# Kernel tuning notes

Measured on AMD Instinct MI355X. Metric: run time of the kernel, lower is better.

## Reference

```python
import jax, jax.numpy as jnp
import numpy as np

B, T, D, H, HD, E, F, K = 512, 32, 512, 16, 32, 4, 2048, 2
EPS = 1e-5

def gelu_gpt2(x):
    c = np.sqrt(2.0 / np.pi).astype(np.float32)
    return 0.5 * x * (1.0 + jnp.tanh(c * (x + 0.044715 * x ** 3)))

def layernorm(x, g, b):
    m = jnp.mean(x, axis=-1, keepdims=True)
    v = jnp.mean((x - m) ** 2, axis=-1, keepdims=True)
    return (x - m) * jax.lax.rsqrt(v + EPS) * g + b

def setup_inputs() -> dict:
    key = jax.random.key(0)
    ks = jax.random.split(key, 12)
    s = 0.02
    return {
        "x": jax.random.normal(ks[0], (B, T, D), jnp.float32),
        "ln1_g": jnp.ones((D,), jnp.float32), "ln1_b": jnp.zeros((D,), jnp.float32),
        "wq": jax.random.normal(ks[1], (H, D, HD), jnp.float32) * s,
        "wk": jax.random.normal(ks[2], (H, D, HD), jnp.float32) * s,
        "wv": jax.random.normal(ks[3], (H, D, HD), jnp.float32) * s,
        "w_proj": jax.random.normal(ks[4], (D, D), jnp.float32) * s,
        "b_proj": jnp.zeros((D,), jnp.float32),
        "ln2_g": jnp.ones((D,), jnp.float32), "ln2_b": jnp.zeros((D,), jnp.float32),
        "w_gate": jax.random.normal(ks[5], (D, E), jnp.float32) * s,
        "w1": jax.random.normal(ks[6], (E, D, F), jnp.float32) * s,
        "b1": jnp.zeros((E, F), jnp.float32),
        "w2": jax.random.normal(ks[7], (E, F, D), jnp.float32) * s,
        "b2": jnp.zeros((E, D), jnp.float32),
    }

def reference(x, ln1_g, ln1_b, wq, wk, wv, w_proj, b_proj, ln2_g, ln2_b, w_gate, w1, b1, w2, b2):
    # --- multi-head causal attention (dropout = eval-mode identity) ---
    h = layernorm(x, ln1_g, ln1_b)                       # [B,T,D]
    q = jnp.einsum('btd,hde->bhte', h, wq)
    k = jnp.einsum('btd,hde->bhte', h, wk)
    v = jnp.einsum('btd,hde->bhte', h, wv)
    # NOTE: original scales by 1/sqrt(n_embd), not head_size
    wei = jnp.einsum('bhte,bhse->bhts', q, k) / jnp.sqrt(jnp.float32(D))
    mask = jnp.tril(jnp.ones((T, T), bool))
    wei = jnp.where(mask, wei, -jnp.inf)
    wei = jax.nn.softmax(wei, axis=-1)
    att = jnp.einsum('bhts,bhse->bhte', wei, v)          # [B,H,T,HD]
    att = att.transpose(0, 2, 1, 3).reshape(B, T, D)     # concat heads
    x = x + att @ w_proj + b_proj
    # --- mixture of experts FFN ---
    h2 = layernorm(x, ln2_g, ln2_b).reshape(-1, D)       # [N,D]
    logits = h2 @ w_gate                                  # [N,E] raw gate output
    # faithful to original: scalar mean over all logits
    ep = jnp.mean(logits)
    bal_loss = ep * jnp.log(ep + 0.1)
    w_top, sel = jax.lax.top_k(logits, K)                # [N,K]
    w_top = jax.nn.softmax(w_top, axis=-1)
    combine = jnp.sum(w_top[:, :, None] * jax.nn.one_hot(sel, E, dtype=x.dtype), axis=1)  # [N,E]
    mid = gelu_gpt2(jnp.einsum('nd,edf->nef', h2, w1) + b1)   # [N,E,F]
    eout = jnp.einsum('nef,efd->ned', mid, w2) + b2           # [N,E,D]
    moe = jnp.einsum('ne,ned->nd', combine, eout).reshape(B, T, D)
    return (x + moe, bal_loss)
```

## Files before the change

### kernel.cpp

```cpp
#include <hip/hip_runtime.h>

typedef unsigned short ushort;
typedef unsigned int   uint;
typedef short bf16x8 __attribute__((ext_vector_type(8)));
typedef float f32x4  __attribute__((ext_vector_type(4)));

__device__ __forceinline__ float bf2f(ushort u){
  union { uint u; float f; } c; c.u = ((uint)u) << 16; return c.f;
}
__device__ __forceinline__ ushort f2bf(float f){
  union { float f; uint u; } c; c.f = f;
  return (ushort)((c.u + 0x7fffu + ((c.u >> 16) & 1u)) >> 16);
}
__device__ __forceinline__ float wredsum(float v){
  #pragma unroll
  for (int off = 32; off > 0; off >>= 1) v += __shfl_xor(v, off);
  return v;
}
__device__ __forceinline__ void gload16(const void* g, void* l){
  __builtin_amdgcn_global_load_lds((__attribute__((address_space(1))) void*)(void*)g,
                                   (__attribute__((address_space(3))) void*)l, 16, 0, 0);
}

template<bool SPLIT>
__global__ __launch_bounds__(256) void transpose_to_bf16(
    const float* __restrict__ src, ushort* __restrict__ dhi, ushort* __restrict__ dlo,
    int R, int C)
{
  __shared__ float tile[32][33];
  size_t zoff = (size_t)blockIdx.z * R * C;
  src += zoff; dhi += zoff; if (SPLIT) dlo += zoff;
  int c0 = blockIdx.x * 32, r0 = blockIdx.y * 32;
  int tx = threadIdx.x & 31, ty = threadIdx.x >> 5;
  #pragma unroll
  for (int i = 0; i < 32; i += 8)
    tile[ty + i][tx] = src[(size_t)(r0 + ty + i) * C + (c0 + tx)];
  __syncthreads();
  #pragma unroll
  for (int i = 0; i < 32; i += 8){
    float v = tile[tx][ty + i];
    ushort hi = f2bf(v);
    dhi[(size_t)(c0 + ty + i) * R + (r0 + tx)] = hi;
    if constexpr (SPLIT)
      dlo[(size_t)(c0 + ty + i) * R + (r0 + tx)] = f2bf(v - bf2f(hi));
  }
}

__global__ __launch_bounds__(256) void ln_split(
    const float* __restrict__ x, const float* __restrict__ g, const float* __restrict__ b,
    ushort* __restrict__ hhi, ushort* __restrict__ hlo)
{
  int w = threadIdx.x >> 6, lane = threadIdx.x & 63;
  int row = blockIdx.x * 4 + w;
  const float* xr = x + (size_t)row * 512;
  int d = lane * 8;
  float4 a0 = *(const float4*)(xr + d);
  float4 a1 = *(const float4*)(xr + d + 4);
  float v[8] = {a0.x,a0.y,a0.z,a0.w,a1.x,a1.y,a1.z,a1.w};
  float s = 0.f;
  #pragma unroll
  for (int j = 0; j < 8; j++) s += v[j];
  s = wredsum(s);
  float mean = s * (1.f/512.f);
  float q = 0.f;
  #pragma unroll
  for (int j = 0; j < 8; j++){ float t = v[j] - mean; q += t*t; }
  q = wredsum(q);
  float rstd = rsqrtf(q * (1.f/512.f) + 1e-5f);
  ushort hu[8], lu[8];
  #pragma unroll
  for (int j = 0; j < 8; j++){
    float h = (v[j] - mean) * rstd * g[d+j] + b[d+j];
    ushort hi = f2bf(h);
    hu[j] = hi;
    lu[j] = f2bf(h - bf2f(hi));
  }
  uint4 oh, ol;
  oh.x = (uint)hu[0] | ((uint)hu[1]<<16); oh.y = (uint)hu[2] | ((uint)hu[3]<<16);
  oh.z = (uint)hu[4] | ((uint)hu[5]<<16); oh.w = (uint)hu[6] | ((uint)hu[7]<<16);
  ol.x = (uint)lu[0] | ((uint)lu[1]<<16); ol.y = (uint)lu[2] | ((uint)lu[3]<<16);
  ol.z = (uint)lu[4] | ((uint)lu[5]<<16); ol.w = (uint)lu[6] | ((uint)lu[7]<<16);
  *(uint4*)(hhi + (size_t)row*512 + d) = oh;
  *(uint4*)(hlo + (size_t)row*512 + d) = ol;
}

template<int EP>
__global__ __launch_bounds__(256) void gemm_bt(
    const ushort* __restrict__ A, const ushort* __restrict__ Alo,
    const ushort* __restrict__ B, const ushort* __restrict__ Blo,
    int M, int N, int K,
    float* __restrict__ outF,
    const float* __restrict__ bias, const float* __restrict__ resid)
{
  __shared__ __align__(16) ushort As[2][128*32];
  __shared__ __align__(16) ushort Bs[2][128*32];
  const int tid  = threadIdx.x;
  const int lane = tid & 63;
  const int w    = tid >> 6;
  const int wm   = w >> 1, wn = w & 1;
  const int bm   = blockIdx.x, bn = blockIdx.y;

  const int    srow = w*16 + (lane >> 2);
  const int    scol = (lane & 3) * 8;
  const size_t aoff = (size_t)(bm*128 + srow) * K + scol;
  const size_t boff = (size_t)(bn*128 + srow) * K + scol;
  const int lbase0 = (w*16) * 32;
  const int lbase1 = (64 + w*16) * 32;

  f32x4 acc[4][4];
  #pragma unroll
  for (int i = 0; i < 4; i++)
    #pragma unroll
    for (int j = 0; j < 4; j++) acc[i][j] = f32x4{0.f,0.f,0.f,0.f};

  const int nk = K >> 5;
  for (int kt = 0; kt < nk; ++kt) {
    const size_t ko = (size_t)kt * 32;
    gload16(A + aoff + ko,               &As[0][lbase0]);
    gload16(A + aoff + (size_t)64*K + ko,&As[0][lbase1]);
    gload16(B + boff + ko,               &Bs[0][lbase0]);
    gload16(B + boff + (size_t)64*K + ko,&Bs[0][lbase1]);
    gload16(Alo + aoff + ko,               &As[1][lbase0]);
    gload16(Alo + aoff + (size_t)64*K + ko,&As[1][lbase1]);
    gload16(Blo + boff + ko,               &Bs[1][lbase0]);
    gload16(Blo + boff + (size_t)64*K + ko,&Bs[1][lbase1]);
    __syncthreads();

    bf16x8 ah[4], bh[4], al[4], bl[4];
    const int kk = (lane >> 4) * 8;
    const int ar = wm*64 + (lane & 15);
    const int br = wn*64 + (lane & 15);
    #pragma unroll
    for (int i = 0; i < 4; i++){
      ah[i] = *(const bf16x8*)&As[0][(ar + i*16)*32 + kk];
      bh[i] = *(const bf16x8*)&Bs[0][(br + i*16)*32 + kk];
      al[i] = *(const bf16x8*)&As[1][(ar + i*16)*32 + kk];
      bl[i] = *(const bf16x8*)&Bs[1][(br + i*16)*32 + kk];
    }
    #pragma unroll
    for (int i = 0; i < 4; i++)
      #pragma unroll
      for (int j = 0; j < 4; j++){
        acc[i][j] = __builtin_amdgcn_mfma_f32_16x16x32_bf16(ah[i], bh[j], acc[i][j], 0,0,0);
        acc[i][j] = __builtin_amdgcn_mfma_f32_16x16x32_bf16(ah[i], bl[j], acc[i][j], 0,0,0);
        acc[i][j] = __builtin_amdgcn_mfma_f32_16x16x32_bf16(al[i], bh[j], acc[i][j], 0,0,0);
      }
    __syncthreads();
  }

  const int r0 = bm*128 + wm*64;
  const int c0 = bn*128 + wn*64;
  const int cl = lane & 15;
  const int rl = (lane >> 4) * 4;
  #pragma unroll
  for (int i = 0; i < 4; i++){
    #pragma unroll
    for (int r = 0; r < 4; r++){
      const int row = r0 + i*16 + rl + r;
      #pragma unroll
      for (int j = 0; j < 4; j++){
        const int col = c0 + j*16 + cl;
        float v = acc[i][j][r];
        size_t idx = (size_t)row * N + col;
        if constexpr (EP == 0) outF[idx] = v;
        else                   outF[idx] = v + bias[col] + resid[idx];
      }
    }
  }
}

__global__ __launch_bounds__(256) void gemm_w1(
    const ushort* __restrict__ A, const ushort* __restrict__ Ball,
    const float* __restrict__ biasAll, ushort* __restrict__ midOut,
    const int* __restrict__ list, const int* __restrict__ seg)
{
  constexpr int K = 512, N = 2048, NBN = 16;
  __shared__ __align__(16) ushort LB[128*132];
  const int tid = threadIdx.x, lane = tid & 63, w = tid >> 6;
  const int wm = w >> 1, wn = w & 1;

  const int nloc = gridDim.x >> 3;
  const int lid  = (blockIdx.x & 7) * nloc + (blockIdx.x >> 3);
  const int bm   = lid / NBN, bn = lid % NBN;
  if (bm >= seg[4]) return;
  int e = 0;
  while (bm >= seg[e+1]) e++;
  const int ltile = bm - seg[e];
  const int* listE = list + e*16384;

  const int jrows = w * 32;
  const int lrow  = lane >> 3;
  const int lgcol = (((lane & 7) ^ lrow)) * 8;

  size_t asrc[4], bsrc[4];
  const ushort* Bm = Ball + (size_t)e * N * K;
  #pragma unroll
  for (int j = 0; j < 4; j++){
    int ar8 = jrows + j*8 + lrow;
    int tok = listE[ltile*128 + ar8];
    asrc[j] = (size_t)tok * K + lgcol;
    bsrc[j] = (size_t)(bn*128 + ar8) * K + lgcol;
  }

  f32x4 acc[4][4];
  #pragma unroll
  for (int i = 0; i < 4; i++)
    #pragma unroll
    for (int j = 0; j < 4; j++) acc[i][j] = f32x4{0.f,0.f,0.f,0.f};

  const int ar = wm*64 + (lane & 15);
  const int br = wn*64 + (lane & 15);
  const int rsw = lane & 7;

  #pragma unroll
  for (int kt = 0; kt < (K >> 6); ++kt){
    const size_t k0 = (size_t)kt * 64;
    #pragma unroll
    for (int j = 0; j < 4; j++){
      gload16(A  + asrc[j] + k0, &LB[(jrows + j*8)*64]);
      gload16(Bm + bsrc[j] + k0, &LB[8192 + (jrows + j*8)*64]);
    }
    __syncthreads();
    #pragma unroll
    for (int ks = 0; ks < 2; ++ks){
      const int g    = ks*4 + (lane >> 4);
      const int goff = (g ^ rsw) * 8;
      bf16x8 af[4], bfr[4];
      #pragma unroll
      for (int i = 0; i < 4; i++){
        af[i]  = *(const bf16x8*)&LB[(ar + i*16)*64 + goff];
        bfr[i] = *(const bf16x8*)&LB[8192 + (br + i*16)*64 + goff];
      }
      #pragma unroll
      for (int i = 0; i < 4; i++)
        #pragma unroll
        for (int j = 0; j < 4; j++)
          acc[i][j] = __builtin_amdgcn_mfma_f32_16x16x32_bf16(af[i], bfr[j], acc[i][j], 0,0,0);
    }
    __syncthreads();
  }

  const int cl = lane & 15;
  const int rl = (lane >> 4) * 4;
  float bj[4];
  #pragma unroll
  for (int j = 0; j < 4; j++)
    bj[j] = biasAll[e*N + bn*128 + wn*64 + j*16 + cl];
  #pragma unroll
  for (int i = 0; i < 4; i++){
    #pragma unroll
    for (int j = 0; j < 4; j++){
      const int cc = wn*64 + j*16 + cl;
      #pragma unroll
      for (int r = 0; r < 4; r++){
        const int rloc = wm*64 + i*16 + rl + r;
        float t = acc[i][j][r] + bj[j];
        float u2 = 1.5957691216057308f * (t + 0.044715f * t*t*t);
        float ex = __expf(u2);
        float gl = t - t * __builtin_amdgcn_rcpf(ex + 1.f);
        LB[rloc*132 + cc] = f2bf(gl);
      }
    }
  }
  __syncthreads();
  const int ch = tid & 15;
  #pragma unroll
  for (int it = 0; it < 8; ++it){
    const int rr = (tid >> 4) + it*16;
    bf16x8 v = *(const bf16x8*)&LB[rr*132 + ch*8];
    *(bf16x8*)&midOut[(size_t)(bm*128 + rr)*2048 + bn*128 + ch*8] = v;
  }
}

__global__ __launch_bounds__(256) void gemm_w2(
    const ushort* __restrict__ mid, const ushort* __restrict__ Ball,
    const float* __restrict__ biasAll, ushort* __restrict__ eout,
    const int* __restrict__ seg)
{
  constexpr int K = 2048, N = 512, NBN = 4;
  __shared__ __align__(16) ushort LB[4*128*64];
  const int tid = threadIdx.x, lane = tid & 63, w = tid >> 6;
  const int wm = w >> 1, wn = w & 1;

  const int nloc = gridDim.x >> 3;
  const int lid  = (blockIdx.x & 7) * nloc + (blockIdx.x >> 3);
  const int bm   = lid / NBN, bn = lid % NBN;
  if (bm >= seg[4]) return;
  int e = 0;
  while (bm >= seg[e+1]) e++;

  const int jrows = w * 32;
  const int lrow  = lane >> 3;
  const int lgcol = (((lane & 7) ^ lrow)) * 8;

  size_t asrc[4], bsrc[4];
  const ushort* Bm = Ball + (size_t)e * N * K;
  #pragma unroll
  for (int j = 0; j < 4; j++){
    int ar8 = jrows + j*8 + lrow;
    asrc[j] = (size_t)(bm*128 + ar8) * K + lgcol;
    bsrc[j] = (size_t)(bn*128 + ar8) * K + lgcol;
  }

  f32x4 acc[4][4];
  #pragma unroll
  for (int i = 0; i < 4; i++)
    #pragma unroll
    for (int j = 0; j < 4; j++) acc[i][j] = f32x4{0.f,0.f,0.f,0.f};

  constexpr int nk = K >> 6;

  #pragma unroll
  for (int j = 0; j < 4; j++){
    gload16(mid + asrc[j], &LB[(jrows + j*8)*64]);
    gload16(Bm  + bsrc[j], &LB[16384 + (jrows + j*8)*64]);
  }
  __syncthreads();

  const int ar = wm*64 + (lane & 15);
  const int br = wn*64 + (lane & 15);
  const int rsw = lane & 7;

  for (int kt = 0; kt < nk; ++kt){
    const int cur = kt & 1;
    const int curA = cur * 8192;
    const int nxtA = (cur ^ 1) * 8192;
    if (kt + 1 < nk){
      const size_t k0 = (size_t)(kt + 1) * 64;
      #pragma unroll
      for (int j = 0; j < 4; j++){
        gload16(mid + asrc[j] + k0, &LB[nxtA + (jrows + j*8)*64]);
        gload16(Bm  + bsrc[j] + k0, &LB[16384 + nxtA + (jrows + j*8)*64]);
      }
    }
    #pragma unroll
    for (int ks = 0; ks < 2; ++ks){
      const int g    = ks*4 + (lane >> 4);
      const int goff = (g ^ rsw) * 8;
      bf16x8 af[4], bfr[4];
      #pragma unroll
      for (int i = 0; i < 4; i++){
        af[i]  = *(const bf16x8*)&LB[curA + (ar + i*16)*64 + goff];
        bfr[i] = *(const bf16x8*)&LB[16384 + curA + (br + i*16)*64 + goff];
      }
      #pragma unroll
      for (int i = 0; i < 4; i++)
        #pragma unroll
        for (int j = 0; j < 4; j++)
          acc[i][j] = __builtin_amdgcn_mfma_f32_16x16x32_bf16(af[i], bfr[j], acc[i][j], 0,0,0);
    }
    __syncthreads();
  }

  const int cl = lane & 15;
  const int rl = (lane >> 4) * 4;
  float bj[4];
  #pragma unroll
  for (int j = 0; j < 4; j++)
    bj[j] = biasAll[e*N + bn*128 + wn*64 + j*16 + cl];
  #pragma unroll
  for (int i = 0; i < 4; i++){
    #pragma unroll
    for (int j = 0; j < 4; j++){
      const int cc = wn*64 + j*16 + cl;
      #pragma unroll
      for (int r = 0; r < 4; r++){
        const int rloc = wm*64 + i*16 + rl + r;
        LB[rloc*132 + cc] = f2bf(acc[i][j][r] + bj[j]);
      }
    }
  }
  __syncthreads();
  const int ch = tid & 15;
  #pragma unroll
  for (int it = 0; it < 8; ++it){
    const int rr = (tid >> 4) + it*16;
    bf16x8 v = *(const bf16x8*)&LB[rr*132 + ch*8];
    *(bf16x8*)&eout[(size_t)(bm*128 + rr)*512 + bn*128 + ch*8] = v;
  }
}

__global__ __launch_bounds__(256) void moe_combine(
    const ushort* __restrict__ eout, const int2* __restrict__ rowSlots,
    const float2* __restrict__ wts, float* __restrict__ out)
{
  int w = threadIdx.x >> 6, lane = threadIdx.x & 63;
  int row = blockIdx.x * 4 + w;
  int2 rs = rowSlots[row];
  float2 wv = wts[row];
  int d = lane * 8;
  uint4 u0 = *(const uint4*)(eout + (size_t)rs.x*512 + d);
  uint4 u1 = *(const uint4*)(eout + (size_t)rs.y*512 + d);
  float* op = out + (size_t)row*512 + d;
  float4 o0 = *(float4*)op;
  float4 o1 = *(float4*)(op + 4);
  o0.x += wv.x*bf2f((ushort)u0.x)        + wv.y*bf2f((ushort)u1.x);
  o0.y += wv.x*bf2f((ushort)(u0.x>>16))  + wv.y*bf2f((ushort)(u1.x>>16));
  o0.z += wv.x*bf2f((ushort)u0.y)        + wv.y*bf2f((ushort)u1.y);
  o0.w += wv.x*bf2f((ushort)(u0.y>>16))  + wv.y*bf2f((ushort)(u1.y>>16));
  o1.x += wv.x*bf2f((ushort)u0.z)        + wv.y*bf2f((ushort)u1.z);
  o1.y += wv.x*bf2f((ushort)(u0.z>>16))  + wv.y*bf2f((ushort)(u1.z>>16));
  o1.z += wv.x*bf2f((ushort)u0.w)        + wv.y*bf2f((ushort)u1.w);
  o1.w += wv.x*bf2f((ushort)(u0.w>>16))  + wv.y*bf2f((ushort)(u1.w>>16));
  *(float4*)op       = o0;
  *(float4*)(op + 4) = o1;
}

__global__ __launch_bounds__(64) void attn32(
    const float* __restrict__ qkv, ushort* __restrict__ atthi, ushort* __restrict__ attlo)
{
  int bh = blockIdx.x; int b = bh >> 4, h = bh & 15;
  __shared__ float qs[32][33], ks[32][33], vs[32][33], ps[32][33];
  int lane = threadIdx.x;
  int t = lane >> 1, cb = (lane & 1) * 16;
  const float* src = qkv + (size_t)(b*32 + t)*1536 + h*32 + cb;
  #pragma unroll
  for (int j = 0; j < 16; j += 4){
    float4 q4 = *(const float4*)(src + j);
    float4 k4 = *(const float4*)(src + 512 + j);
    float4 v4 = *(const float4*)(src + 1024 + j);
    qs[t][cb+j]=q4.x; qs[t][cb+j+1]=q4.y; qs[t][cb+j+2]=q4.z; qs[t][cb+j+3]=q4.w;
    ks[t][cb+j]=k4.x; ks[t][cb+j+1]=k4.y; ks[t][cb+j+2]=k4.z; ks[t][cb+j+3]=k4.w;
    vs[t][cb+j]=v4.x; vs[t][cb+j+1]=v4.y; vs[t][cb+j+2]=v4.z; vs[t][cb+j+3]=v4.w;
  }
  __syncthreads();
  const float scale = 0.044194173824159216f;
  float sc[16];
  #pragma unroll
  for (int j = 0; j < 16; j++){
    int c = cb + j;
    if (c <= t) {
      float d = 0.f;
      #pragma unroll
      for (int i = 0; i < 32; i++) d += qs[t][i] * ks[c][i];
      sc[j] = d * scale;
    } else sc[j] = -1e30f;
  }
  float mx = -1e30f;
  #pragma unroll
  for (int j = 0; j < 16; j++) mx = fmaxf(mx, sc[j]);
  mx = fmaxf(mx, __shfl_xor(mx, 1));
  float p[16], sum = 0.f;
  #pragma unroll
  for (int j = 0; j < 16; j++){
    int c = cb + j;
    if (c <= t) { p[j] = expf(sc[j] - mx); sum += p[j]; } else p[j] = 0.f;
  }
  sum += __shfl_xor(sum, 1);
  float inv = 1.f / sum;
  #pragma unroll
  for (int j = 0; j < 16; j++) ps[t][cb+j] = p[j] * inv;
  __syncthreads();
  float o[16];
  #pragma unroll
  for (int j = 0; j < 16; j++) o[j] = 0.f;
  for (int s2 = 0; s2 <= t; ++s2){
    float wv = ps[t][s2];
    #pragma unroll
    for (int j = 0; j < 16; j++) o[j] += wv * vs[s2][cb+j];
  }
  size_t base = (size_t)(b*32 + t)*512 + h*32 + cb;
  ushort hu[16], lu[16];
  #pragma unroll
  for (int j = 0; j < 16; j++){
    ushort hi = f2bf(o[j]);
    hu[j] = hi; lu[j] = f2bf(o[j] - bf2f(hi));
  }
  uint4 oh0, oh1, ol0, ol1;
  oh0.x=(uint)hu[0]|((uint)hu[1]<<16);  oh0.y=(uint)hu[2]|((uint)hu[3]<<16);
  oh0.z=(uint)hu[4]|((uint)hu[5]<<16);  oh0.w=(uint)hu[6]|((uint)hu[7]<<16);
  oh1.x=(uint)hu[8]|((uint)hu[9]<<16);  oh1.y=(uint)hu[10]|((uint)hu[11]<<16);
  oh1.z=(uint)hu[12]|((uint)hu[13]<<16);oh1.w=(uint)hu[14]|((uint)hu[15]<<16);
  ol0.x=(uint)lu[0]|((uint)lu[1]<<16);  ol0.y=(uint)lu[2]|((uint)lu[3]<<16);
  ol0.z=(uint)lu[4]|((uint)lu[5]<<16);  ol0.w=(uint)lu[6]|((uint)lu[7]<<16);
  ol1.x=(uint)lu[8]|((uint)lu[9]<<16);  ol1.y=(uint)lu[10]|((uint)lu[11]<<16);
  ol1.z=(uint)lu[12]|((uint)lu[13]<<16);ol1.w=(uint)lu[14]|((uint)lu[15]<<16);
  *(uint4*)(atthi + base)     = oh0;  *(uint4*)(atthi + base + 8) = oh1;
  *(uint4*)(attlo + base)     = ol0;  *(uint4*)(attlo + base + 8) = ol1;
}

__global__ __launch_bounds__(256) void ln2_gate(
    const float* __restrict__ x1, const float* __restrict__ g, const float* __restrict__ b,
    const float* __restrict__ wgate, ushort* __restrict__ h2,
    int* __restrict__ selp, float2* __restrict__ wts,
    int* __restrict__ blockCnt, float* __restrict__ partials)
{
  __shared__ float wsumLds[4];
  __shared__ int   selLds[4];
  int w = threadIdx.x >> 6, lane = threadIdx.x & 63;
  int row = blockIdx.x * 4 + w;
  const float* xr = x1 + (size_t)row * 512;
  int d = lane * 8;
  float4 a0 = *(const float4*)(xr + d);
  float4 a1 = *(const float4*)(xr + d + 4);
  float v[8] = {a0.x,a0.y,a0.z,a0.w,a1.x,a1.y,a1.z,a1.w};
  float s = 0.f;
  #pragma unroll
  for (int j = 0; j < 8; j++) s += v[j];
  s = wredsum(s);
  float mean = s * (1.f/512.f);
  float q = 0.f;
  #pragma unroll
  for (int j = 0; j < 8; j++){ float t = v[j] - mean; q += t*t; }
  q = wredsum(q);
  float rstd = rsqrtf(q * (1.f/512.f) + 1e-5f);
  float acc0=0.f, acc1=0.f, acc2=0.f, acc3=0.f;
  ushort hu[8];
  #pragma unroll
  for (int j = 0; j < 8; j++){
    float h = (v[j] - mean) * rstd * g[d+j] + b[d+j];
    hu[j] = f2bf(h);
    float4 wgv = *(const float4*)(wgate + (size_t)(d+j)*4);
    acc0 += h * wgv.x; acc1 += h * wgv.y; acc2 += h * wgv.z; acc3 += h * wgv.w;
  }
  uint4 oh;
  oh.x=(uint)hu[0]|((uint)hu[1]<<16); oh.y=(uint)hu[2]|((uint)hu[3]<<16);
  oh.z=(uint)hu[4]|((uint)hu[5]<<16); oh.w=(uint)hu[6]|((uint)hu[7]<<16);
  *(uint4*)(h2 + (size_t)row*512 + d) = oh;
  acc0 = wredsum(acc0); acc1 = wredsum(acc1); acc2 = wredsum(acc2); acc3 = wredsum(acc3);
  if (lane == 0){
    float l[4] = {acc0, acc1, acc2, acc3};
    int i0 = 0;
    for (int e = 1; e < 4; e++) if (l[e] > l[i0]) i0 = e;
    int i1 = -1;
    for (int e = 0; e < 4; e++){ if (e == i0) continue; if (i1 < 0 || l[e] > l[i1]) i1 = e; }
    float e1 = expf(l[i1] - l[i0]);
    float w1v = e1 / (1.f + e1), w0v = 1.f / (1.f + e1);
    int packed = i0 | (i1 << 8);
    selp[row] = packed;
    wts[row]  = make_float2(w0v, w1v);
    selLds[w] = packed;
    wsumLds[w] = l[0] + l[1] + l[2] + l[3];
  }
  __syncthreads();
  if (threadIdx.x < 4){
    int e = threadIdx.x, c = 0;
    #pragma unroll
    for (int i = 0; i < 4; i++){
      int sp = selLds[i];
      c += ((sp & 0xff) == e) + (((sp >> 8) & 0xff) == e);
    }
    blockCnt[e*4096 + blockIdx.x] = c;
  }
  if (threadIdx.x == 0)
    partials[blockIdx.x] = wsumLds[0] + wsumLds[1] + wsumLds[2] + wsumLds[3];
}

__global__ __launch_bounds__(256) void scan_offsets(
    const int* __restrict__ blockCnt, int* __restrict__ blockOff,
    int* __restrict__ cnt, int* __restrict__ seg)
{
  __shared__ int cntL[4];
  int w = threadIdx.x >> 6, lane = threadIdx.x & 63;
  const int* src = blockCnt + w*4096;
  int* dst = blockOff + w*4096;
  int off = 0;
  for (int i = 0; i < 4096; i += 64){
    int v = src[i + lane];
    int orig = v;
    #pragma unroll
    for (int dlt = 1; dlt < 64; dlt <<= 1){
      int t = __shfl_up(v, dlt);
      if (lane >= dlt) v += t;
    }
    dst[i + lane] = off + v - orig;
    off += __shfl(v, 63);
  }
  if (lane == 0){ cnt[w] = off; cntL[w] = off; }
  __syncthreads();
  if (threadIdx.x == 0){
    int t = 0;
    for (int e = 0; e < 4; e++){ seg[e] = t; t += (cntL[e] + 127) >> 7; }
    seg[4] = t;
  }
}

__global__ __launch_bounds__(256) void route_write(
    const int* __restrict__ selp, const int* __restrict__ blockOff,
    const int* __restrict__ seg, int* __restrict__ list, int2* __restrict__ rowSlots)
{
  int row = blockIdx.x * 256 + threadIdx.x;
  int g = row & ~3;
  int b = row >> 2;
  int my = selp[row];
  int e0 = my & 0xff, e1 = (my >> 8) & 0xff;
  int r0 = 0, r1 = 0;
  for (int r = g; r < row; ++r){
    int sp = selp[r];
    int a = sp & 0xff, c = (sp >> 8) & 0xff;
    r0 += (a == e0) + (c == e0);
    r1 += (a == e1) + (c == e1);
  }
  int slot0 = blockOff[e0*4096 + b] + r0;
  int slot1 = blockOff[e1*4096 + b] + r1;
  list[e0*16384 + slot0] = row;
  list[e1*16384 + slot1] = row;
  rowSlots[row] = make_int2(seg[e0]*128 + slot0, seg[e1]*128 + slot1);
}

__global__ __launch_bounds__(256) void gate_reduce(
    const float* __restrict__ partials, int n, float* __restrict__ out)
{
  __shared__ float ws4[4];
  float s = 0.f;
  for (int i = threadIdx.x; i < n; i += 256) s += partials[i];
  s = wredsum(s);
  if ((threadIdx.x & 63) == 0) ws4[threadIdx.x >> 6] = s;
  __syncthreads();
  if (threadIdx.x == 0){
    float tot = ws4[0] + ws4[1] + ws4[2] + ws4[3];
    float ep = tot * (1.f/65536.f);
    out[0] = ep * logf(ep + 0.1f);
  }
}

extern "C" void kernel_launch(void* const* d_in, const int* in_sizes, int n_in,
                              void* d_out, int out_size, void* d_ws, size_t ws_size,
                              hipStream_t stream)
{
  const float* x     = (const float*)d_in[0];
  const float* ln1g  = (const float*)d_in[1];
  const float* ln1b  = (const float*)d_in[2];
  const float* wq    = (const float*)d_in[3];
  const float* wk    = (const float*)d_in[4];
  const float* wv    = (const float*)d_in[5];
  const float* wproj = (const float*)d_in[6];
  const float* bproj = (const float*)d_in[7];
  const float* ln2g  = (const float*)d_in[8];
  const float* ln2b  = (const float*)d_in[9];
  const float* wgate = (const float*)d_in[10];
  const float* w1    = (const float*)d_in[11];
  const float* b1    = (const float*)d_in[12];
  const float* w2    = (const float*)d_in[13];
  const float* b2    = (const float*)d_in[14];
  float* out = (float*)d_out;

  char* ws = (char*)d_ws;
  ushort* hHi   = (ushort*)(ws + 0);
  ushort* hLo   = (ushort*)(ws + 16777216);
  ushort* qkvTh = (ushort*)(ws + 33554432);
  ushort* qkvTl = (ushort*)(ws + 35127296);
  ushort* pTh   = (ushort*)(ws + 36700160);
  ushort* pTl   = (ushort*)(ws + 37224448);
  float*  qkvF  = (float*)(ws + 37748736);
  ushort* attHi = (ushort*)(ws + 138412032);
  ushort* attLo = (ushort*)(ws + 155189248);
  ushort* mid   = (ushort*)(ws + 0);
  ushort* eout  = (ushort*)(ws + 137183744);
  ushort* h2    = (ushort*)(ws + 171966464);
  ushort* w1T   = (ushort*)(ws + 188743680);
  ushort* w2T   = (ushort*)(ws + 197132288);
  char* rb = ws + 136314880;
  int*    cnt      = (int*)   (rb + 0);
  int*    seg      = (int*)   (rb + 256);
  int*    list     = (int*)   (rb + 512);
  int2*   rowSlots = (int2*)  (rb + 262656);
  float*  partials = (float*) (rb + 524800);
  int*    selp     = (int*)   (rb + 541184);
  float2* wts      = (float2*)(rb + 606720);
  int*    blockCnt = (int*)   (rb + 737792);
  int*    blockOff = (int*)   (rb + 803328);

  transpose_to_bf16<true ><<<dim3(1,16,16), 256, 0, stream>>>(wq,    qkvTh,          qkvTl,          512, 32);
  transpose_to_bf16<true ><<<dim3(1,16,16), 256, 0, stream>>>(wk,    qkvTh + 262144, qkvTl + 262144, 512, 32);
  transpose_to_bf16<true ><<<dim3(1,16,16), 256, 0, stream>>>(wv,    qkvTh + 524288, qkvTl + 524288, 512, 32);
  transpose_to_bf16<true ><<<dim3(16,16,1), 256, 0, stream>>>(wproj, pTh,            pTl,            512, 512);
  transpose_to_bf16<false><<<dim3(64,16,4), 256, 0, stream>>>(w1,    w1T,            nullptr,        512, 2048);
  transpose_to_bf16<false><<<dim3(16,64,4), 256, 0, stream>>>(w2,    w2T,            nullptr,        2048, 512);

  ln_split<<<dim3(4096), 256, 0, stream>>>(x, ln1g, ln1b, hHi, hLo);

  gemm_bt<0><<<dim3(128,12), 256, 0, stream>>>(hHi, hLo, qkvTh, qkvTl,
      16384, 1536, 512, qkvF, nullptr, nullptr);

  attn32<<<dim3(8192), 64, 0, stream>>>(qkvF, attHi, attLo);

  gemm_bt<1><<<dim3(128,4), 256, 0, stream>>>(attHi, attLo, pTh, pTl,
      16384, 512, 512, out, bproj, x);

  (void)hipMemsetAsync(list, 0, 4*16384*sizeof(int), stream);
  ln2_gate<<<dim3(4096), 256, 0, stream>>>(out, ln2g, ln2b, wgate, h2, selp, wts, blockCnt, partials);
  scan_offsets<<<dim3(1), 256, 0, stream>>>(blockCnt, blockOff, cnt, seg);
  route_write<<<dim3(64), 256, 0, stream>>>(selp, blockOff, seg, list, rowSlots);
  gate_reduce<<<dim3(1), 256, 0, stream>>>(partials, 4096, out + 8388608);

  gemm_w1<<<dim3(4160), 256, 0, stream>>>(h2,  w1T, b1, mid,  list, seg);
  gemm_w2<<<dim3(1040), 256, 0, stream>>>(mid, w2T, b2, eout, seg);
  moe_combine<<<dim3(4096), 256, 0, stream>>>(eout, rowSlots, wts, out);
}
```

Measured before the change: 467.0 us.

## Merge small launches and single-buffer the w2 expert GEMM

The three Q/K/V weight transposes become one launch of a dedicated transpose_qkv kernel, and the balance-loss reduction is folded into scan_offsets, so gate_reduce and its launch go away. Separately, gemm_w2 drops its LDS double buffer for a single buffer with load, sync, compute each K step. That halves its shared-memory use and may raise occupancy, but the global loads no longer overlap with the MFMA work.

```diff
diff --git a/kernel.cpp b/kernel.cpp
--- a/kernel.cpp
+++ b/kernel.cpp
@@ -43,6 +43,32 @@
     dhi[(size_t)(c0 + ty + i) * R + (r0 + tx)] = hi;
     if constexpr (SPLIT)
       dlo[(size_t)(c0 + ty + i) * R + (r0 + tx)] = f2bf(v - bf2f(hi));
+  }
+}
+
+__global__ __launch_bounds__(256) void transpose_qkv(
+    const float* __restrict__ wq, const float* __restrict__ wk, const float* __restrict__ wv,
+    ushort* __restrict__ dhi, ushort* __restrict__ dlo)
+{
+  __shared__ float tile[32][33];
+  int z = blockIdx.z;
+  int which = z >> 4, h = z & 15;
+  const float* src = (which == 0) ? wq : (which == 1) ? wk : wv;
+  size_t soff = (size_t)h * 512 * 32;
+  size_t doff = (size_t)which * 262144 + soff;
+  src += soff;
+  int r0 = blockIdx.y * 32;
+  int tx = threadIdx.x & 31, ty = threadIdx.x >> 5;
+  #pragma unroll
+  for (int i = 0; i < 32; i += 8)
+    tile[ty + i][tx] = src[(size_t)(r0 + ty + i) * 32 + tx];
+  __syncthreads();
+  #pragma unroll
+  for (int i = 0; i < 32; i += 8){
+    float v = tile[tx][ty + i];
+    ushort hi = f2bf(v);
+    dhi[doff + (size_t)(ty + i) * 512 + (r0 + tx)] = hi;
+    dlo[doff + (size_t)(ty + i) * 512 + (r0 + tx)] = f2bf(v - bf2f(hi));
   }
 }
 
@@ -278,7 +304,7 @@
     const int* __restrict__ seg)
 {
   constexpr int K = 2048, N = 512, NBN = 4;
-  __shared__ __align__(16) ushort LB[4*128*64];
+  __shared__ __align__(16) ushort LB[128*132];
   const int tid = threadIdx.x, lane = tid & 63, w = tid >> 6;
   const int wm = w >> 1, wn = w & 1;
 
@@ -308,31 +334,18 @@
     #pragma unroll
     for (int j = 0; j < 4; j++) acc[i][j] = f32x4{0.f,0.f,0.f,0.f};
 
-  constexpr int nk = K >> 6;
-
-  #pragma unroll
-  for (int j = 0; j < 4; j++){
-    gload16(mid + asrc[j], &LB[(jrows + j*8)*64]);
-    gload16(Bm  + bsrc[j], &LB[16384 + (jrows + j*8)*64]);
-  }
-  __syncthreads();
-
   const int ar = wm*64 + (lane & 15);
   const int br = wn*64 + (lane & 15);
   const int rsw = lane & 7;
 
-  for (int kt = 0; kt < nk; ++kt){
-    const int cur = kt & 1;
-    const int curA = cur * 8192;
-    const int nxtA = (cur ^ 1) * 8192;
-    if (kt + 1 < nk){
-      const size_t k0 = (size_t)(kt + 1) * 64;
-      #pragma unroll
-      for (int j = 0; j < 4; j++){
-        gload16(mid + asrc[j] + k0, &LB[nxtA + (jrows + j*8)*64]);
-        gload16(Bm  + bsrc[j] + k0, &LB[16384 + nxtA + (jrows + j*8)*64]);
-      }
-    }
+  for (int kt = 0; kt < (K >> 6); ++kt){
+    const size_t k0 = (size_t)kt * 64;
+    #pragma unroll
+    for (int j = 0; j < 4; j++){
+      gload16(mid + asrc[j] + k0, &LB[(jrows + j*8)*64]);
+      gload16(Bm  + bsrc[j] + k0, &LB[8192 + (jrows + j*8)*64]);
+    }
+    __syncthreads();
     #pragma unroll
     for (int ks = 0; ks < 2; ++ks){
       const int g    = ks*4 + (lane >> 4);
@@ -340,8 +353,8 @@
       bf16x8 af[4], bfr[4];
       #pragma unroll
       for (int i = 0; i < 4; i++){
-        af[i]  = *(const bf16x8*)&LB[curA + (ar + i*16)*64 + goff];
-        bfr[i] = *(const bf16x8*)&LB[16384 + curA + (br + i*16)*64 + goff];
+        af[i]  = *(const bf16x8*)&LB[(ar + i*16)*64 + goff];
+        bfr[i] = *(const bf16x8*)&LB[8192 + (br + i*16)*64 + goff];
       }
       #pragma unroll
       for (int i = 0; i < 4; i++)
@@ -548,9 +561,11 @@
 
 __global__ __launch_bounds__(256) void scan_offsets(
     const int* __restrict__ blockCnt, int* __restrict__ blockOff,
-    int* __restrict__ cnt, int* __restrict__ seg)
+    int* __restrict__ cnt, int* __restrict__ seg,
+    const float* __restrict__ partials, float* __restrict__ lossOut)
 {
   __shared__ int cntL[4];
+  __shared__ float ws4[4];
   int w = threadIdx.x >> 6, lane = threadIdx.x & 63;
   const int* src = blockCnt + w*4096;
   int* dst = blockOff + w*4096;
@@ -572,6 +587,16 @@
     int t = 0;
     for (int e = 0; e < 4; e++){ seg[e] = t; t += (cntL[e] + 127) >> 7; }
     seg[4] = t;
+  }
+  float s = 0.f;
+  for (int i = threadIdx.x; i < 4096; i += 256) s += partials[i];
+  s = wredsum(s);
+  if ((threadIdx.x & 63) == 0) ws4[threadIdx.x >> 6] = s;
+  __syncthreads();
+  if (threadIdx.x == 0){
+    float tot = ws4[0] + ws4[1] + ws4[2] + ws4[3];
+    float ep = tot * (1.f/65536.f);
+    lossOut[0] = ep * logf(ep + 0.1f);
   }
 }
 
@@ -596,22 +621,6 @@
   list[e0*16384 + slot0] = row;
   list[e1*16384 + slot1] = row;
   rowSlots[row] = make_int2(seg[e0]*128 + slot0, seg[e1]*128 + slot1);
-}
-
-__global__ __launch_bounds__(256) void gate_reduce(
-    const float* __restrict__ partials, int n, float* __restrict__ out)
-{
-  __shared__ float ws4[4];
-  float s = 0.f;
-  for (int i = threadIdx.x; i < n; i += 256) s += partials[i];
-  s = wredsum(s);
-  if ((threadIdx.x & 63) == 0) ws4[threadIdx.x >> 6] = s;
-  __syncthreads();
-  if (threadIdx.x == 0){
-    float tot = ws4[0] + ws4[1] + ws4[2] + ws4[3];
-    float ep = tot * (1.f/65536.f);
-    out[0] = ep * logf(ep + 0.1f);
-  }
 }
 
 extern "C" void kernel_launch(void* const* d_in, const int* in_sizes, int n_in,
@@ -661,12 +670,10 @@
   int*    blockCnt = (int*)   (rb + 737792);
   int*    blockOff = (int*)   (rb + 803328);
 
-  transpose_to_bf16<true ><<<dim3(1,16,16), 256, 0, stream>>>(wq,    qkvTh,          qkvTl,          512, 32);
-  transpose_to_bf16<true ><<<dim3(1,16,16), 256, 0, stream>>>(wk,    qkvTh + 262144, qkvTl + 262144, 512, 32);
-  transpose_to_bf16<true ><<<dim3(1,16,16), 256, 0, stream>>>(wv,    qkvTh + 524288, qkvTl + 524288, 512, 32);
-  transpose_to_bf16<true ><<<dim3(16,16,1), 256, 0, stream>>>(wproj, pTh,            pTl,            512, 512);
-  transpose_to_bf16<false><<<dim3(64,16,4), 256, 0, stream>>>(w1,    w1T,            nullptr,        512, 2048);
-  transpose_to_bf16<false><<<dim3(16,64,4), 256, 0, stream>>>(w2,    w2T,            nullptr,        2048, 512);
+  transpose_qkv<<<dim3(1,16,48), 256, 0, stream>>>(wq, wk, wv, qkvTh, qkvTl);
+  transpose_to_bf16<true ><<<dim3(16,16,1), 256, 0, stream>>>(wproj, pTh, pTl, 512, 512);
+  transpose_to_bf16<false><<<dim3(64,16,4), 256, 0, stream>>>(w1, w1T, nullptr, 512, 2048);
+  transpose_to_bf16<false><<<dim3(16,64,4), 256, 0, stream>>>(w2, w2T, nullptr, 2048, 512);
 
   ln_split<<<dim3(4096), 256, 0, stream>>>(x, ln1g, ln1b, hHi, hLo);
 
@@ -680,9 +687,8 @@
 
   (void)hipMemsetAsync(list, 0, 4*16384*sizeof(int), stream);
   ln2_gate<<<dim3(4096), 256, 0, stream>>>(out, ln2g, ln2b, wgate, h2, selp, wts, blockCnt, partials);
-  scan_offsets<<<dim3(1), 256, 0, stream>>>(blockCnt, blockOff, cnt, seg);
+  scan_offsets<<<dim3(1), 256, 0, stream>>>(blockCnt, blockOff, cnt, seg, partials, out + 8388608);
   route_write<<<dim3(64), 256, 0, stream>>>(selp, blockOff, seg, list, rowSlots);
-  gate_reduce<<<dim3(1), 256, 0, stream>>>(partials, 4096, out + 8388608);
 
   gemm_w1<<<dim3(4160), 256, 0, stream>>>(h2,  w1T, b1, mid,  list, seg);
   gemm_w2<<<dim3(1040), 256, 0, stream>>>(mid, w2T, b2, eout, seg);
```

Result: slower. 486.9 us (+4.3%).
